# Kernel optimization log

Measured on AMD Instinct MI355X. Metric: run time of the kernel, lower is better.

## Reference

```python
import jax, jax.numpy as jnp
import numpy as np
from jax.scipy.special import logsumexp

B, T, K = 1024, 512, 64
START, STOP = 0, K - 1
NEG = -10000.0


def setup_inputs() -> dict:
    key = jax.random.key(0)
    k1, k2, k3 = jax.random.split(key, 3)
    feats = jax.random.normal(k1, (B, T, K), dtype=jnp.float32)
    tags = jax.random.randint(k2, (B, T), 0, K)
    transitions = jax.random.normal(k3, (K, K), dtype=jnp.float32)
    # never transition INTO start, never transition OUT of stop
    transitions = transitions.at[START, :].set(NEG).at[:, STOP].set(NEG)
    return {"feats": feats, "tags": tags, "transitions": transitions}


def reference(feats, tags, transitions):
    feats_t = jnp.swapaxes(feats, 0, 1)  # [T, B, K]
    alpha0 = jnp.full((B, K), NEG, dtype=feats.dtype).at[:, START].set(0.0)

    # ---- CRF forward algorithm (log partition) ----
    def fwd_step(alpha, emit):  # alpha [B,K(prev)], emit [B,K(next)]
        scores = alpha[:, None, :] + transitions[None, :, :]  # [B, next, prev]
        return logsumexp(scores, axis=2) + emit, None

    alphaT, _ = jax.lax.scan(fwd_step, alpha0, feats_t)
    fwd_score = logsumexp(alphaT + transitions[STOP][None, :], axis=1)  # [B]

    # ---- gold path score ----
    start_col = jnp.full((B, 1), START, dtype=tags.dtype)
    tags_ext = jnp.concatenate([start_col, tags], axis=1)  # [B, T+1]
    prev, nxt = tags_ext[:, :-1], tags_ext[:, 1:]
    trans_sc = transitions[nxt, prev].sum(axis=1)
    emit_sc = jnp.take_along_axis(feats, nxt[:, :, None], axis=2)[..., 0].sum(axis=1)
    gold_score = trans_sc + emit_sc + transitions[STOP, tags_ext[:, -1]]  # [B]

    nll = fwd_score - gold_score  # [B]

    # ---- Viterbi decode (batched; original loops over one sequence) ----
    def vit_step(alpha, emit):
        scores = alpha[:, None, :] + transitions[None, :, :]  # [B, next, prev]
        bp = jnp.argmax(scores, axis=2)  # [B, K]
        return jnp.max(scores, axis=2) + emit, bp

    v_alpha, bps = jax.lax.scan(vit_step, alpha0, feats_t)  # bps [T, B, K]
    term = v_alpha + transitions[STOP][None, :]
    best_last = jnp.argmax(term, axis=1)  # [B]
    vit_score = jnp.max(term, axis=1)  # [B]

    def back_step(tag, bp):  # tag [B] = tag at time t; bp [B, K]
        prev_tag = jnp.take_along_axis(bp, tag[:, None], axis=1)[:, 0]
        return prev_tag, tag

    _, path_rev = jax.lax.scan(back_step, best_last, bps, reverse=True)  # [T, B]
    best_path = jnp.swapaxes(path_rev, 0, 1)  # [B, T]

    return nll, vit_score, best_path
```

## Files before the change

kernel.cpp:

```cpp
#include <hip/hip_runtime.h>

#define BB 1024
#define TT 512
#define KK 64
#define NEGV -10000.0f

typedef _Float16 h2 __attribute__((ext_vector_type(2)));

#if defined(__has_builtin)
#if __has_builtin(__builtin_amdgcn_fdot2)
#define HAVE_FDOT2 1
#endif
#endif

static __device__ __forceinline__ float dot2_acc(h2 a, h2 b, float c) {
#ifdef HAVE_FDOT2
    return __builtin_amdgcn_fdot2(a, b, c, false);
#else
    return fmaf((float)a.x, (float)b.x, fmaf((float)a.y, (float)b.y, c));
#endif
}

static __device__ __forceinline__ h2 bc_h2(float f) {
    return __builtin_bit_cast(h2, f);
}

__global__ __launch_bounds__(256) void gold_kernel(const float* __restrict__ feats,
                                                   const int* __restrict__ tags,
                                                   const float* __restrict__ trans,
                                                   float* __restrict__ gold) {
    const int wv = threadIdx.x >> 6;
    const int lane = threadIdx.x & 63;
    const int b = blockIdx.x * 4 + wv;
    const int* tg = tags + (size_t)b * TT;
    float acc = 0.f;
#pragma unroll
    for (int i = 0; i < TT / 64; ++i) {
        int t = lane + i * 64;
        int nxt = tg[t];
        int prv = (t == 0) ? 0 : tg[t - 1];
        acc += trans[nxt * KK + prv] + feats[((size_t)b * TT + t) * KK + nxt];
    }
    if (lane == 0) acc += trans[(KK - 1) * KK + tg[TT - 1]];
#pragma unroll
    for (int d = 1; d < 64; d <<= 1) acc += __shfl_xor(acc, d);
    if (lane == 0) gold[b] = acc;
}

__global__ __launch_bounds__(128) void crf_kernel(const float* __restrict__ feats,
                                                  const float* __restrict__ trans,
                                                  const float* __restrict__ gold,
                                                  float* __restrict__ out) {
    __shared__ unsigned char bp[TT][KK];
    __shared__ __align__(16) float wa_buf[KK];
    __shared__ __align__(16) _Float16 ea_buf[KK];
    __shared__ unsigned char path_buf[TT];
    __shared__ float sh_fscore;
    __shared__ float sh_bvv;

    const int b = blockIdx.x;
    const int wv = threadIdx.x >> 6;
    const int lane = threadIdx.x & 63;
    const int role = wv ^ (b & 1);

    const float* fb = feats + (size_t)b * TT * KK + lane;

    if (role == 0) {
        h2 Er_pk[32];
        {
            const float4* trow = reinterpret_cast<const float4*>(trans + lane * KK);
#pragma unroll
            for (int i = 0; i < 16; ++i) {
                float4 v = trow[i];
                h2 lo, hi;
                lo.x = (_Float16)__expf(v.x); lo.y = (_Float16)__expf(v.y);
                hi.x = (_Float16)__expf(v.z); hi.y = (_Float16)__expf(v.w);
                Er_pk[2 * i] = lo;
                Er_pk[2 * i + 1] = hi;
            }
        }
        const float t63 = trans[(KK - 1) * KK + lane];

        float a = (lane == 0) ? 0.f : NEGV;
        float ref = 0.f;
        float f_next = fb[0];

        for (int t = 0; t < TT; ++t) {
            const float f_cur = f_next;
            {
                int tn = (t + 1 < TT) ? (t + 1) : (TT - 1);
                f_next = fb[(size_t)tn * KK];
            }
            float x = fminf(a - ref, 11.0f);
            ea_buf[lane] = (_Float16)__expf(x);

            float s0 = 0.f, s1 = 0.f, s2 = 0.f, s3 = 0.f;
            const float4* eb = reinterpret_cast<const float4*>(ea_buf);
#pragma unroll
            for (int q = 0; q < 8; ++q) {
                float4 e4 = eb[q];
                s0 = dot2_acc(bc_h2(e4.x), Er_pk[4 * q + 0], s0);
                s1 = dot2_acc(bc_h2(e4.y), Er_pk[4 * q + 1], s1);
                s2 = dot2_acc(bc_h2(e4.z), Er_pk[4 * q + 2], s2);
                s3 = dot2_acc(bc_h2(e4.w), Er_pk[4 * q + 3], s3);
            }
            float s = (s0 + s1) + (s2 + s3);
            float a_new = __logf(s) + ref + f_cur;
            ref = __shfl(a_new, 8) + 3.0f;
            a = a_new;
        }

        float v = a + t63;
        float mm = v;
#pragma unroll
        for (int d = 32; d; d >>= 1) mm = fmaxf(mm, __shfl_xor(mm, d));
        float es = __expf(v - mm);
#pragma unroll
        for (int d = 32; d; d >>= 1) es += __shfl_xor(es, d);
        float fscore = mm + __logf(es);
        if (lane == 0) sh_fscore = fscore;
    } else {
        float tr[KK];
        {
            const float4* trow = reinterpret_cast<const float4*>(trans + lane * KK);
#pragma unroll
            for (int i = 0; i < KK / 4; ++i) {
                float4 v = trow[i];
                tr[4 * i + 0] = v.x; tr[4 * i + 1] = v.y;
                tr[4 * i + 2] = v.z; tr[4 * i + 3] = v.w;
            }
        }
        const float t63 = trans[(KK - 1) * KK + lane];

        float w = (lane == 0) ? 0.f : NEGV;
        wa_buf[lane] = w;
        float f_next = fb[0];

        for (int t = 0; t < TT; ++t) {
            const float f_cur = f_next;
            {
                int tn = (t + 1 < TT) ? (t + 1) : (TT - 1);
                f_next = fb[(size_t)tn * KK];
            }

            float gm[8];
#pragma unroll
            for (int gi = 0; gi < 8; ++gi) gm[gi] = -3.4e38f;

            const float4* wb = reinterpret_cast<const float4*>(wa_buf);
#pragma unroll
            for (int q = 0; q < 16; ++q) {
                float4 w4 = wb[q];
                float v0 = w4.x + tr[4 * q + 0];
                float v1 = w4.y + tr[4 * q + 1];
                float v2 = w4.z + tr[4 * q + 2];
                float v3 = w4.w + tr[4 * q + 3];
                int g = q >> 1;
                gm[g] = fmaxf(fmaxf(gm[g], v0), v1);
                gm[g] = fmaxf(fmaxf(gm[g], v2), v3);
            }

            float m = fmaxf(fmaxf(fmaxf(gm[0], gm[1]), fmaxf(gm[2], gm[3])),
                            fmaxf(fmaxf(gm[4], gm[5]), fmaxf(gm[6], gm[7])));
            int g = 0;
#pragma unroll
            for (int j = 7; j >= 0; --j)
                if (gm[j] == m) g = j;
            const int base = g * 8;
            const float4* wam = reinterpret_cast<const float4*>(wa_buf + base);
            float4 wa0 = wam[0], wa1 = wam[1];
            const float4* trg = reinterpret_cast<const float4*>(trans + lane * KK + base);
            float4 tg0 = trg[0], tg1 = trg[1];
            int bpv = base;
            {
                float vv;
                vv = wa1.w + tg1.w; if (vv == m) bpv = base + 7;
                vv = wa1.z + tg1.z; if (vv == m) bpv = base + 6;
                vv = wa1.y + tg1.y; if (vv == m) bpv = base + 5;
                vv = wa1.x + tg1.x; if (vv == m) bpv = base + 4;
                vv = wa0.w + tg0.w; if (vv == m) bpv = base + 3;
                vv = wa0.z + tg0.z; if (vv == m) bpv = base + 2;
                vv = wa0.y + tg0.y; if (vv == m) bpv = base + 1;
                vv = wa0.x + tg0.x; if (vv == m) bpv = base + 0;
            }
            bp[t][lane] = (unsigned char)bpv;
            float w_new = m + f_cur;
            wa_buf[lane] = w_new;
            w = w_new;
        }

        float tv = w + t63;
        float bvv = tv;
        int bidx = lane;
#pragma unroll
        for (int d = 1; d < 64; d <<= 1) {
            float ov = __shfl_xor(bvv, d);
            int oi = __shfl_xor(bidx, d);
            bool take = (ov > bvv) || (ov == bvv && oi < bidx);
            bvv = take ? ov : bvv;
            bidx = take ? oi : bidx;
        }

        if (lane == 0) {
            sh_bvv = bvv;
            int cur = bidx;
            for (int t = TT - 1; t >= 0; --t) {
                path_buf[t] = (unsigned char)cur;
                cur = bp[t][cur];
            }
        }
    }

    __syncthreads();

    if (threadIdx.x == 0) {
        out[b] = sh_fscore - gold[b];
        out[BB + b] = sh_bvv;
    }
#pragma unroll
    for (int i = 0; i < TT / 128; ++i) {
        int t = threadIdx.x + i * 128;
        out[2 * BB + (size_t)b * TT + t] = (float)path_buf[t];
    }
}

extern "C" void kernel_launch(void* const* d_in, const int* in_sizes, int n_in,
                              void* d_out, int out_size, void* d_ws, size_t ws_size,
                              hipStream_t stream) {
    const float* feats = (const float*)d_in[0];
    const int* tags = (const int*)d_in[1];
    const float* trans = (const float*)d_in[2];
    float* out = (float*)d_out;
    float* gold = (float*)d_ws;

    gold_kernel<<<BB / 4, 256, 0, stream>>>(feats, tags, trans, gold);
    crf_kernel<<<BB, 128, 0, stream>>>(feats, trans, gold, out);
}
```

Before: 387.8 us.

## Move backpointers to global workspace, defer argmax, parallelize backtrace via shuffles

Backpointers go to a global workspace buffer (when it is large enough) instead of 32KB of LDS, which shrinks LDS per block and allows more resident blocks. The Viterbi backpointer argmax for step t is deferred into step t+1 so it overlaps the next max reduction, and feats are prefetched two steps ahead. The forward recurrence's stabilizing reference is delayed by two steps to take the shuffle off the critical path. Backtrace now runs wave-wide with shuffles over chunks of 16 steps instead of a serial lane-0 loop, and the block-wide sync is removed. The cost is extra global traffic for backpointers (32MB written and read back) and added register pressure.

```diff
diff --git a/kernel.cpp b/kernel.cpp
--- a/kernel.cpp
+++ b/kernel.cpp
@@ -47,16 +47,15 @@
     if (lane == 0) gold[b] = acc;
 }
 
+template <bool GBP>
 __global__ __launch_bounds__(128) void crf_kernel(const float* __restrict__ feats,
                                                   const float* __restrict__ trans,
                                                   const float* __restrict__ gold,
+                                                  unsigned char* __restrict__ bp_g,
                                                   float* __restrict__ out) {
-    __shared__ unsigned char bp[TT][KK];
     __shared__ __align__(16) float wa_buf[KK];
     __shared__ __align__(16) _Float16 ea_buf[KK];
-    __shared__ unsigned char path_buf[TT];
-    __shared__ float sh_fscore;
-    __shared__ float sh_bvv;
+    __shared__ unsigned char bp_l[GBP ? 4 : TT * KK];
 
     const int b = blockIdx.x;
     const int wv = threadIdx.x >> 6;
@@ -82,31 +81,44 @@
         const float t63 = trans[(KK - 1) * KK + lane];
 
         float a = (lane == 0) ? 0.f : NEGV;
-        float ref = 0.f;
-        float f_next = fb[0];
+        float refUse = 0.f, refMid = 6.f, refNew = 12.f;
+
+        float f0 = fb[0];
+        float f1 = fb[KK];
+        const float* fp = fb + 2 * KK;
 
         for (int t = 0; t < TT; ++t) {
-            const float f_cur = f_next;
-            {
-                int tn = (t + 1 < TT) ? (t + 1) : (TT - 1);
-                f_next = fb[(size_t)tn * KK];
-            }
-            float x = fminf(a - ref, 11.0f);
+            const float f_cur = f0;
+            f0 = f1;
+            f1 = *fp;
+            if (t + 3 < TT) fp += KK;
+
+            float x = fminf(a - refUse, 11.0f);
             ea_buf[lane] = (_Float16)__expf(x);
 
+            const float4* eb = reinterpret_cast<const float4*>(ea_buf);
             float s0 = 0.f, s1 = 0.f, s2 = 0.f, s3 = 0.f;
-            const float4* eb = reinterpret_cast<const float4*>(ea_buf);
+            float s4 = 0.f, s5 = 0.f, s6 = 0.f, s7 = 0.f;
 #pragma unroll
             for (int q = 0; q < 8; ++q) {
                 float4 e4 = eb[q];
-                s0 = dot2_acc(bc_h2(e4.x), Er_pk[4 * q + 0], s0);
-                s1 = dot2_acc(bc_h2(e4.y), Er_pk[4 * q + 1], s1);
-                s2 = dot2_acc(bc_h2(e4.z), Er_pk[4 * q + 2], s2);
-                s3 = dot2_acc(bc_h2(e4.w), Er_pk[4 * q + 3], s3);
-            }
-            float s = (s0 + s1) + (s2 + s3);
-            float a_new = __logf(s) + ref + f_cur;
-            ref = __shfl(a_new, 8) + 3.0f;
+                float acc = 0.f;
+                acc = dot2_acc(bc_h2(e4.x), Er_pk[4 * q + 0], acc);
+                acc = dot2_acc(bc_h2(e4.y), Er_pk[4 * q + 1], acc);
+                acc = dot2_acc(bc_h2(e4.z), Er_pk[4 * q + 2], acc);
+                acc = dot2_acc(bc_h2(e4.w), Er_pk[4 * q + 3], acc);
+                switch (q) {
+                    case 0: s0 = acc; break; case 1: s1 = acc; break;
+                    case 2: s2 = acc; break; case 3: s3 = acc; break;
+                    case 4: s4 = acc; break; case 5: s5 = acc; break;
+                    case 6: s6 = acc; break; case 7: s7 = acc; break;
+                }
+            }
+            float s = ((s0 + s1) + (s2 + s3)) + ((s4 + s5) + (s6 + s7));
+            float a_new = __logf(s) + refUse + f_cur;
+            refUse = refMid;
+            refMid = refNew;
+            refNew = __shfl(a_new, 8) + 5.0f;
             a = a_new;
         }
 
@@ -118,7 +130,7 @@
 #pragma unroll
         for (int d = 32; d; d >>= 1) es += __shfl_xor(es, d);
         float fscore = mm + __logf(es);
-        if (lane == 0) sh_fscore = fscore;
+        if (lane == 0) out[b] = fscore - gold[b];
     } else {
         float tr[KK];
         {
@@ -132,16 +144,40 @@
         }
         const float t63 = trans[(KK - 1) * KK + lane];
 
+        unsigned char* bpc = GBP ? (bp_g + (size_t)b * TT * KK + lane) : (bp_l + lane);
+
         float w = (lane == 0) ? 0.f : NEGV;
         wa_buf[lane] = w;
-        float f_next = fb[0];
+
+        float f0 = fb[0];
+        float f1 = fb[KK];
+        const float* fp = fb + 2 * KK;
+
+        float4 p_wa0, p_wa1, p_tg0, p_tg1;
+        float p_m = 0.f;
+        int p_base = 0;
+        unsigned char* bpw = bpc;
 
         for (int t = 0; t < TT; ++t) {
-            const float f_cur = f_next;
-            {
-                int tn = (t + 1 < TT) ? (t + 1) : (TT - 1);
-                f_next = fb[(size_t)tn * KK];
-            }
+            if (t) {
+                int bpv = p_base;
+                float vv;
+                vv = p_wa1.w + p_tg1.w; if (vv == p_m) bpv = p_base + 7;
+                vv = p_wa1.z + p_tg1.z; if (vv == p_m) bpv = p_base + 6;
+                vv = p_wa1.y + p_tg1.y; if (vv == p_m) bpv = p_base + 5;
+                vv = p_wa1.x + p_tg1.x; if (vv == p_m) bpv = p_base + 4;
+                vv = p_wa0.w + p_tg0.w; if (vv == p_m) bpv = p_base + 3;
+                vv = p_wa0.z + p_tg0.z; if (vv == p_m) bpv = p_base + 2;
+                vv = p_wa0.y + p_tg0.y; if (vv == p_m) bpv = p_base + 1;
+                vv = p_wa0.x + p_tg0.x; if (vv == p_m) bpv = p_base + 0;
+                *bpw = (unsigned char)bpv;
+                bpw += KK;
+            }
+
+            const float f_cur = f0;
+            f0 = f1;
+            f1 = *fp;
+            if (t + 3 < TT) fp += KK;
 
             float gm[8];
 #pragma unroll
@@ -167,26 +203,30 @@
             for (int j = 7; j >= 0; --j)
                 if (gm[j] == m) g = j;
             const int base = g * 8;
+
             const float4* wam = reinterpret_cast<const float4*>(wa_buf + base);
-            float4 wa0 = wam[0], wa1 = wam[1];
+            p_wa0 = wam[0];
+            p_wa1 = wam[1];
+            wa_buf[lane] = m + f_cur;
             const float4* trg = reinterpret_cast<const float4*>(trans + lane * KK + base);
-            float4 tg0 = trg[0], tg1 = trg[1];
-            int bpv = base;
-            {
-                float vv;
-                vv = wa1.w + tg1.w; if (vv == m) bpv = base + 7;
-                vv = wa1.z + tg1.z; if (vv == m) bpv = base + 6;
-                vv = wa1.y + tg1.y; if (vv == m) bpv = base + 5;
-                vv = wa1.x + tg1.x; if (vv == m) bpv = base + 4;
-                vv = wa0.w + tg0.w; if (vv == m) bpv = base + 3;
-                vv = wa0.z + tg0.z; if (vv == m) bpv = base + 2;
-                vv = wa0.y + tg0.y; if (vv == m) bpv = base + 1;
-                vv = wa0.x + tg0.x; if (vv == m) bpv = base + 0;
-            }
-            bp[t][lane] = (unsigned char)bpv;
-            float w_new = m + f_cur;
-            wa_buf[lane] = w_new;
-            w = w_new;
+            p_tg0 = trg[0];
+            p_tg1 = trg[1];
+            p_m = m;
+            p_base = base;
+            w = m + f_cur;
+        }
+        {
+            int bpv = p_base;
+            float vv;
+            vv = p_wa1.w + p_tg1.w; if (vv == p_m) bpv = p_base + 7;
+            vv = p_wa1.z + p_tg1.z; if (vv == p_m) bpv = p_base + 6;
+            vv = p_wa1.y + p_tg1.y; if (vv == p_m) bpv = p_base + 5;
+            vv = p_wa1.x + p_tg1.x; if (vv == p_m) bpv = p_base + 4;
+            vv = p_wa0.w + p_tg0.w; if (vv == p_m) bpv = p_base + 3;
+            vv = p_wa0.z + p_tg0.z; if (vv == p_m) bpv = p_base + 2;
+            vv = p_wa0.y + p_tg0.y; if (vv == p_m) bpv = p_base + 1;
+            vv = p_wa0.x + p_tg0.x; if (vv == p_m) bpv = p_base + 0;
+            *bpw = (unsigned char)bpv;
         }
 
         float tv = w + t63;
@@ -200,27 +240,24 @@
             bvv = take ? ov : bvv;
             bidx = take ? oi : bidx;
         }
-
-        if (lane == 0) {
-            sh_bvv = bvv;
-            int cur = bidx;
-            for (int t = TT - 1; t >= 0; --t) {
-                path_buf[t] = (unsigned char)cur;
-                cur = bp[t][cur];
-            }
-        }
-    }
-
-    __syncthreads();
-
-    if (threadIdx.x == 0) {
-        out[b] = sh_fscore - gold[b];
-        out[BB + b] = sh_bvv;
-    }
-#pragma unroll
-    for (int i = 0; i < TT / 128; ++i) {
-        int t = threadIdx.x + i * 128;
-        out[2 * BB + (size_t)b * TT + t] = (float)path_buf[t];
+        if (lane == 0) out[BB + b] = bvv;
+
+        float* outp = out + 2 * BB + (size_t)b * TT;
+        int cur = bidx;
+        float my = 0.f;
+        for (int tb = TT - 16; tb >= 0; tb -= 16) {
+            int r[16];
+#pragma unroll
+            for (int j = 0; j < 16; ++j)
+                r[j] = GBP ? (int)bpc[(size_t)(tb + j) * KK]
+                           : (int)bp_l[(tb + j) * KK + lane];
+#pragma unroll
+            for (int j = 15; j >= 0; --j) {
+                my = (lane == ((tb + j) & 63)) ? (float)cur : my;
+                cur = __shfl(r[j], cur);
+            }
+            if ((tb & 63) == 0) outp[tb + lane] = my;
+        }
     }
 }
 
@@ -232,7 +269,14 @@
     const float* trans = (const float*)d_in[2];
     float* out = (float*)d_out;
     float* gold = (float*)d_ws;
+    unsigned char* bp_g = (unsigned char*)d_ws + 4096;
 
     gold_kernel<<<BB / 4, 256, 0, stream>>>(feats, tags, trans, gold);
-    crf_kernel<<<BB, 128, 0, stream>>>(feats, trans, gold, out);
-}
+
+    const size_t need = (size_t)BB * TT * KK + 4096;
+    if (ws_size >= need) {
+        crf_kernel<true><<<BB, 128, 0, stream>>>(feats, trans, gold, bp_g, out);
+    } else {
+        crf_kernel<false><<<BB, 128, 0, stream>>>(feats, trans, gold, nullptr, out);
+    }
+}
```

New measurement: 512.8 us. +32.2%, slower.
